# Optimization experiments

Hardware: AMD Instinct MI355X
Metric: run time of the kernel (lower is better)

Reference implementation:

```python
import jax, jax.numpy as jnp
import numpy as np

B, S, E = 2, 256, 512
H, DH = 8, 64            # heads, head_dim = E // H
TC = 768                 # tokens already resident in the paged cache


def setup_inputs() -> dict:
    key = jax.random.key(0)
    ks = jax.random.split(key, 8)
    scale = 1.0 / np.sqrt(E)
    return {
        "x": jax.random.normal(ks[0], (B, S, E), dtype=jnp.float32),
        # cache is stored token-major flattened over heads: [B, TC*H, DH]
        "k_cache": jax.random.normal(ks[1], (B, TC * H, DH), dtype=jnp.float32),
        "v_cache": jax.random.normal(ks[2], (B, TC * H, DH), dtype=jnp.float32),
        "Wq": jax.random.normal(ks[3], (E, E), dtype=jnp.float32) * scale,
        "bq": jnp.zeros((E,), dtype=jnp.float32),
        "Wk": jax.random.normal(ks[4], (E, E), dtype=jnp.float32) * scale,
        "bk": jnp.zeros((E,), dtype=jnp.float32),
        "Wv": jax.random.normal(ks[5], (E, E), dtype=jnp.float32) * scale,
        "bv": jnp.zeros((E,), dtype=jnp.float32),
        "Wo": jax.random.normal(ks[6], (E, E), dtype=jnp.float32) * scale,
        "bo": jnp.zeros((E,), dtype=jnp.float32),
    }


def reference(x, k_cache, v_cache, Wq, bq, Wk, bk, Wv, bv, Wo, bo):
    b, s, _ = x.shape
    # projections (torch Linear: y = x @ W.T + b)
    Q = (x @ Wq.T + bq).reshape(b, s, H, DH).transpose(0, 2, 1, 3)       # [B,H,S,DH]
    new_K = (x @ Wk.T + bk).reshape(b, s, H, DH)                         # [B,S,H,DH]
    new_V = (x @ Wv.T + bv).reshape(b, s, H, DH)
    # cache appends per-token [B,H,DH] slices and cats along dim=-2,
    # producing token-major flattened KV of shape [B, T*H, DH]
    K = jnp.concatenate([k_cache, new_K.reshape(b, s * H, DH)], axis=1)  # [B,L,DH]
    V = jnp.concatenate([v_cache, new_V.reshape(b, s * H, DH)], axis=1)
    # broadcasted matmul: Q [B,H,S,DH] against K [B,1,L,DH] -> scores [B,H,S,L]
    scores = jnp.einsum("bhsd,bld->bhsl", Q, K) / np.sqrt(DH).astype(jnp.float32)
    attn = jax.nn.softmax(scores, axis=-1)
    out = jnp.einsum("bhsl,bld->bhsd", attn, V)                          # [B,H,S,DH]
    out = out.transpose(0, 2, 1, 3).reshape(b, s, E)
    return out @ Wo.T + bo
```

## Files before the change

### kernel.cpp

```cpp
#include <hip/hip_runtime.h>
#include <math.h>

#define B_   2
#define LTOT   8192
#define LCACHE 6144
#define LNEW   2048

#define QSCALE (0.125f * 1.44269504088896f)

typedef __attribute__((ext_vector_type(8))) short bf16x8;
typedef __attribute__((ext_vector_type(4))) float f32x4;

__device__ __forceinline__ ushort f2bf(float f) {
    unsigned u = __float_as_uint(f);
    return (ushort)((u + 0x7fffu + ((u >> 16) & 1u)) >> 16);
}
__device__ __forceinline__ void split_hilo(float v, ushort& h, ushort& l) {
    h = f2bf(v);
    l = f2bf(v - __uint_as_float((unsigned)h << 16));
}


__device__ __forceinline__ void convert_slot(
    const float* __restrict__ src, ushort* __restrict__ dh, ushort* __restrict__ dl, int slot)
{
    const int R = slot >> 10, kk = (slot >> 6) & 15, ln = slot & 63;
    const int row = R * 16 + (ln & 15), col = kk * 32 + (ln >> 4) * 8;
    const float4 a  = *reinterpret_cast<const float4*>(src + row * 512 + col);
    const float4 b4 = *reinterpret_cast<const float4*>(src + row * 512 + col + 4);
    ushort4 h0, l0, h1, l1;
    split_hilo(a.x,  h0.x, l0.x); split_hilo(a.y,  h0.y, l0.y);
    split_hilo(a.z,  h0.z, l0.z); split_hilo(a.w,  h0.w, l0.w);
    split_hilo(b4.x, h1.x, l1.x); split_hilo(b4.y, h1.y, l1.y);
    split_hilo(b4.z, h1.z, l1.z); split_hilo(b4.w, h1.w, l1.w);
    *reinterpret_cast<ushort4*>(dh + slot * 8)     = h0;
    *reinterpret_cast<ushort4*>(dh + slot * 8 + 4) = h1;
    *reinterpret_cast<ushort4*>(dl + slot * 8)     = l0;
    *reinterpret_cast<ushort4*>(dl + slot * 8 + 4) = l1;
}

__device__ __forceinline__ void kcache_slot(
    const float* __restrict__ Kc, ushort* __restrict__ Khi, ushort* __restrict__ Klo,
    int b, int slot)
{
    const int key = slot >> 3, g = slot & 7;
    const int h = g >> 2, lg = g & 3;
    const float* src = Kc + ((size_t)b * LCACHE + key) * 64 + g * 8;
    const float4 a  = *reinterpret_cast<const float4*>(src);
    const float4 b4 = *reinterpret_cast<const float4*>(src + 4);
    const int T = key >> 5, r = key & 31;
    const int lr = ((r >> 3) << 2) | (r & 3), st = (r >> 2) & 1;
    const size_t dst = (size_t)b * 524288 + T * 2048 + st * 1024
                     + h * 512 + (((size_t)lg << 4 | lr)) * 8;
    ushort4 h0, l0, h1, l1;
    split_hilo(a.x,  h0.x, l0.x); split_hilo(a.y,  h0.y, l0.y);
    split_hilo(a.z,  h0.z, l0.z); split_hilo(a.w,  h0.w, l0.w);
    split_hilo(b4.x, h1.x, l1.x); split_hilo(b4.y, h1.y, l1.y);
    split_hilo(b4.z, h1.z, l1.z); split_hilo(b4.w, h1.w, l1.w);
    *reinterpret_cast<ushort4*>(Khi + dst)     = h0;
    *reinterpret_cast<ushort4*>(Khi + dst + 4) = h1;
    *reinterpret_cast<ushort4*>(Klo + dst)     = l0;
    *reinterpret_cast<ushort4*>(Klo + dst + 4) = l1;
}

__device__ __forceinline__ void proj8(
    const ushort* __restrict__ AhF, const ushort* __restrict__ AlF,
    const ushort* __restrict__ BhF, const ushort* __restrict__ BlF,
    const float* __restrict__ bias, const int mode, const int bxp, const int byp,
    ushort* __restrict__ d1, ushort* __restrict__ d2, float* __restrict__ df)
{
    const int tid = threadIdx.x;
    const int wv = tid >> 6, lane = tid & 63;
    const int lr = lane & 15, lg = lane >> 4;
    const int m0 = byp * 64 + (wv & 3) * 16;
    const int n0 = bxp * 64 + (wv >> 2) * 32;
    const int mT = m0 >> 4, nT = n0 >> 4;

    f32x4 acc[2];
    acc[0] = (f32x4){0.f, 0.f, 0.f, 0.f};
    acc[1] = (f32x4){0.f, 0.f, 0.f, 0.f};

    const ushort* Ah = AhF + (size_t)nT * 8192 + lane * 8;
    const ushort* Al = AlF + (size_t)nT * 8192 + lane * 8;
    const ushort* Bh = BhF + (size_t)mT * 8192 + lane * 8;
    const ushort* Bl = BlF + (size_t)mT * 8192 + lane * 8;

#pragma unroll 4
    for (int kk = 0; kk < 16; ++kk) {
        bf16x8 ah[2], al[2], bh, bl;
#pragma unroll
        for (int t = 0; t < 2; ++t) {
            ah[t] = *reinterpret_cast<const bf16x8*>(Ah + t * 8192 + kk * 512);
            al[t] = *reinterpret_cast<const bf16x8*>(Al + t * 8192 + kk * 512);
        }
        bh = *reinterpret_cast<const bf16x8*>(Bh + kk * 512);
        bl = *reinterpret_cast<const bf16x8*>(Bl + kk * 512);
        __builtin_amdgcn_s_setprio(1);
#pragma unroll
        for (int ni = 0; ni < 2; ++ni) {
            acc[ni] = __builtin_amdgcn_mfma_f32_16x16x32_bf16(ah[ni], bh, acc[ni], 0, 0, 0);
            acc[ni] = __builtin_amdgcn_mfma_f32_16x16x32_bf16(ah[ni], bl, acc[ni], 0, 0, 0);
            acc[ni] = __builtin_amdgcn_mfma_f32_16x16x32_bf16(al[ni], bh, acc[ni], 0, 0, 0);
        }
        __builtin_amdgcn_s_setprio(0);
    }

#pragma unroll
    for (int ni = 0; ni < 2; ++ni) {
        const int tok = m0 + lr;
        const int e   = n0 + ni * 16 + lg * 4;
        const float4 bb4 = *reinterpret_cast<const float4*>(&bias[e]);
        float v0 = acc[ni].x + bb4.x, v1 = acc[ni].y + bb4.y;
        float v2 = acc[ni].z + bb4.z, v3 = acc[ni].w + bb4.w;
        const int bb = tok >> 8, s = tok & 255;
        if (mode == 0) {
            v0 *= QSCALE; v1 *= QSCALE; v2 *= QSCALE; v3 *= QSCALE;
            ushort4 h, l;
            split_hilo(v0, h.x, l.x); split_hilo(v1, h.y, l.y);
            split_hilo(v2, h.z, l.z); split_hilo(v3, h.w, l.w);
            const size_t off = (size_t)bb * 131072 + s * 512 + e;
            *reinterpret_cast<ushort4*>(d1 + off) = h;
            *reinterpret_cast<ushort4*>(d2 + off) = l;
        } else if (mode == 1) {
            const int key = LCACHE + s * 8 + (e >> 6);
            const int d0 = e & 63;
            const int T = key >> 5, r = key & 31;
            const int klr = ((r >> 3) << 2) | (r & 3), st = (r >> 2) & 1;
            const int h = d0 >> 5, lg2 = (d0 >> 3) & 3, j0 = d0 & 7;
            const size_t dst = (size_t)bb * 524288 + T * 2048 + st * 1024
                             + h * 512 + ((lg2 << 4) | klr) * 8 + j0;
            ushort4 hh, ll;
            split_hilo(v0, hh.x, ll.x); split_hilo(v1, hh.y, ll.y);
            split_hilo(v2, hh.z, ll.z); split_hilo(v3, hh.w, ll.w);
            *reinterpret_cast<ushort4*>(d1 + dst) = hh;
            *reinterpret_cast<ushort4*>(d2 + dst) = ll;
        } else if (mode == 2) {
            const int key = LCACHE + s * 8 + (e >> 6);
            const int Tv = key >> 5;
            const int lg3 = (key & 31) >> 3, j = key & 7;
            const float vals[4] = {v0, v1, v2, v3};
#pragma unroll
            for (int c = 0; c < 4; ++c) {
                const int d = (e & 63) + c;
                const int dt = d >> 4, vlr = d & 15;
                d1[(size_t)bb * 524288 + Tv * 2048 + dt * 512
                   + ((lg3 << 4) | vlr) * 8 + j] = f2bf(vals[c]);
            }
        } else {
            float4 o; o.x = v0; o.y = v1; o.z = v2; o.w = v3;
            *reinterpret_cast<float4*>(df + (size_t)tok * 512 + e) = o;
        }
    }
}

#define ALOAD(kf, lf, vf, t) do {                                                   \
    _Pragma("unroll")                                                               \
    for (int st = 0; st < 2; ++st) {                                                \
        _Pragma("unroll")                                                           \
        for (int h = 0; h < 2; ++h) {                                               \
            kf[st][h] = *reinterpret_cast<const bf16x8*>(kh_p + (t) * 2048 + st * 1024 + h * 512); \
            lf[st][h] = *reinterpret_cast<const bf16x8*>(kl_p + (t) * 2048 + st * 1024 + h * 512); \
        }                                                                           \
    }                                                                               \
    _Pragma("unroll")                                                               \
    for (int dt = 0; dt < 4; ++dt)                                                  \
        vf[dt] = *reinterpret_cast<const bf16x8*>(vt_p + (t) * 2048 + dt * 512);    \
} while (0)

#define ACOMP(kf, lf, vf) do {                                                      \
    f32x4 s0 = {0.f,0.f,0.f,0.f}, s1 = {0.f,0.f,0.f,0.f};                           \
    __builtin_amdgcn_s_setprio(1);                                                  \
    _Pragma("unroll")                                                               \
    for (int h = 0; h < 2; ++h) {                                                   \
        s0 = __builtin_amdgcn_mfma_f32_16x16x32_bf16(kf[0][h], qh[h], s0, 0, 0, 0); \
        s0 = __builtin_amdgcn_mfma_f32_16x16x32_bf16(kf[0][h], ql[h], s0, 0, 0, 0); \
        s0 = __builtin_amdgcn_mfma_f32_16x16x32_bf16(lf[0][h], qh[h], s0, 0, 0, 0); \
        s1 = __builtin_amdgcn_mfma_f32_16x16x32_bf16(kf[1][h], qh[h], s1, 0, 0, 0); \
        s1 = __builtin_amdgcn_mfma_f32_16x16x32_bf16(kf[1][h], ql[h], s1, 0, 0, 0); \
        s1 = __builtin_amdgcn_mfma_f32_16x16x32_bf16(lf[1][h], qh[h], s1, 0, 0, 0); \
    }                                                                               \
    __builtin_amdgcn_s_setprio(0);                                                  \
    float tm = fmaxf(fmaxf(fmaxf(s0.x, s0.y), fmaxf(s0.z, s0.w)),                   \
                     fmaxf(fmaxf(s1.x, s1.y), fmaxf(s1.z, s1.w)));                  \
    tm = fmaxf(tm, __shfl_xor(tm, 16));                                             \
    tm = fmaxf(tm, __shfl_xor(tm, 32));                                             \
    const float mn = fmaxf(m, tm);                                                  \
    const float corr = __builtin_exp2f(m - mn);                                     \
    float p[8];                                                                     \
    p[0] = __builtin_exp2f(s0.x - mn); p[1] = __builtin_exp2f(s0.y - mn);           \
    p[2] = __builtin_exp2f(s0.z - mn); p[3] = __builtin_exp2f(s0.w - mn);           \
    p[4] = __builtin_exp2f(s1.x - mn); p[5] = __builtin_exp2f(s1.y - mn);           \
    p[6] = __builtin_exp2f(s1.z - mn); p[7] = __builtin_exp2f(s1.w - mn);           \
    float ps = ((p[0]+p[1]) + (p[2]+p[3])) + ((p[4]+p[5]) + (p[6]+p[7]));           \
    ps += __shfl_xor(ps, 16);                                                       \
    ps += __shfl_xor(ps, 32);                                                       \
    l = l * corr + ps; m = mn;                                                      \
    union { bf16x8 v; ushort u[8]; } pf;                                            \
    _Pragma("unroll")                                                               \
    for (int j = 0; j < 8; ++j) pf.u[j] = f2bf(p[j]);                               \
    __builtin_amdgcn_s_setprio(1);                                                  \
    _Pragma("unroll")                                                               \
    for (int dt = 0; dt < 4; ++dt) {                                                \
        f32x4 a = acc[dt];                                                          \
        a.x *= corr; a.y *= corr; a.z *= corr; a.w *= corr;                         \
        acc[dt] = __builtin_amdgcn_mfma_f32_16x16x32_bf16(vf[dt], pf.v, a, 0, 0, 0);\
    }                                                                               \
    __builtin_amdgcn_s_setprio(0);                                                  \
} while (0)

__device__ __forceinline__ void gridbarrier(uint* flags, uint* rel, int bar, int bid)
{
    __syncthreads();
    const uint ep = 0x1357A001u + (uint)bar;
    uint* f = flags + bar * 256;
    if (threadIdx.x == 0)
        __hip_atomic_store(f + bid, ep, __ATOMIC_RELEASE, __HIP_MEMORY_SCOPE_AGENT);
    if (bid == 0) {
        if (threadIdx.x < 256) {
            while (__hip_atomic_load(f + threadIdx.x, __ATOMIC_RELAXED,
                                     __HIP_MEMORY_SCOPE_AGENT) != ep)
                __builtin_amdgcn_s_sleep(32);
        }
        __syncthreads();
        if (threadIdx.x == 0)
            __hip_atomic_store(rel + bar, ep, __ATOMIC_RELEASE, __HIP_MEMORY_SCOPE_AGENT);
    }
    if (threadIdx.x == 0) {
        while (__hip_atomic_load(rel + bar, __ATOMIC_RELAXED,
                                 __HIP_MEMORY_SCOPE_AGENT) != ep)
            __builtin_amdgcn_s_sleep(32);
        (void)__hip_atomic_load(f + bid, __ATOMIC_ACQUIRE, __HIP_MEMORY_SCOPE_AGENT);
    }
    __syncthreads();
}

__global__ __launch_bounds__(512, 2) void fused_all(
    const float* __restrict__ x,  const float* __restrict__ Kc,
    const float* __restrict__ Vc,
    const float* __restrict__ Wq, const float* __restrict__ bq,
    const float* __restrict__ Wk, const float* __restrict__ bk,
    const float* __restrict__ Wv, const float* __restrict__ bv,
    const float* __restrict__ Wo, const float* __restrict__ bo,
    float* __restrict__ out,
    ushort* __restrict__ Khi, ushort* __restrict__ Klo, ushort* __restrict__ VtS,
    ushort* __restrict__ Qhi, ushort* __restrict__ Qlo,
    ushort* __restrict__ xh,  ushort* __restrict__ xl,
    ushort* __restrict__ Wqh, ushort* __restrict__ Wql,
    ushort* __restrict__ Wkh, ushort* __restrict__ Wkl,
    ushort* __restrict__ Wvh, ushort* __restrict__ Wvl,
    ushort* __restrict__ Woh, ushort* __restrict__ Wol,
    ushort* __restrict__ Aoh, ushort* __restrict__ Aol,
    uint* __restrict__ gflags, uint* __restrict__ grel)
{
    __shared__ union SM {
        ushort sT[64][68];
        struct { float sAcc[8][16][68]; float sM[8][16]; float sL[8][16]; } a;
    } sm;

    const int bid = blockIdx.x, tid = threadIdx.x;
    const int gid = bid * 512 + tid;

    {
        const int z = gid >> 15, slot = gid & 32767;
        const float* src; ushort* dh; ushort* dl;
        if (z == 0)      { src = x;  dh = xh;  dl = xl;  }
        else if (z == 1) { src = Wq; dh = Wqh; dl = Wql; }
        else if (z == 2) { src = Wk; dh = Wkh; dl = Wkl; }
        else             { src = Wv; dh = Wvh; dl = Wvl; }
        convert_slot(src, dh, dl, slot);
    }
    gridbarrier(gflags, grel, 0, bid);

    if (bid < 192) {
        const int z = bid >> 6, idx = bid & 63;
        const int bxp = idx & 7, byp = idx >> 3;
        if (z == 0)      proj8(Wqh, Wql, xh, xl, bq, 0, bxp, byp, Qhi, Qlo, nullptr);
        else if (z == 1) proj8(Wkh, Wkl, xh, xl, bk, 1, bxp, byp, Khi, Klo, nullptr);
        else             proj8(Wvh, Wvl, xh, xl, bv, 2, bxp, byp, VtS, nullptr, nullptr);
    } else {
        const int lid = (bid - 192) * 512 + tid;
        convert_slot(Wo, Woh, Wol, lid);
#pragma unroll
        for (int k = 0; k < 3; ++k) {
            int slot = lid + k * 32768;
            const int b = slot >= 49152 ? 1 : 0;
            kcache_slot(Kc, Khi, Klo, b, slot - b * 49152);
        }
#pragma unroll
        for (int vt = 0; vt < 3; ++vt) {
            const int tix = (bid - 192) * 3 + vt;
            const int b = tix / 96, kt = tix % 96;
            const int key0 = kt * 64;
            __syncthreads();
#pragma unroll
            for (int it = 0; it < 2; ++it) {
                const int id = it * 512 + tid;
                const int row = id >> 4, c4 = (id & 15) << 2;
                const float4 v = *reinterpret_cast<const float4*>(
                    &Vc[((size_t)b * LCACHE + key0 + row) * 64 + c4]);
                sm.sT[c4+0][row] = f2bf(v.x); sm.sT[c4+1][row] = f2bf(v.y);
                sm.sT[c4+2][row] = f2bf(v.z); sm.sT[c4+3][row] = f2bf(v.w);
            }
            __syncthreads();
            {
                const int s = tid;
                const int Tl = s >> 8, dt = (s >> 6) & 3, ln = s & 63;
                const int lr2 = ln & 15, lg2 = ln >> 4;
                const int kb = Tl * 32 + lg2 * 8;
                ushort4 o0, o1;
                o0.x = sm.sT[dt*16+lr2][kb+0]; o0.y = sm.sT[dt*16+lr2][kb+1];
                o0.z = sm.sT[dt*16+lr2][kb+2]; o0.w = sm.sT[dt*16+lr2][kb+3];
                o1.x = sm.sT[dt*16+lr2][kb+4]; o1.y = sm.sT[dt*16+lr2][kb+5];
                o1.z = sm.sT[dt*16+lr2][kb+6]; o1.w = sm.sT[dt*16+lr2][kb+7];
                const size_t dst = (size_t)b * 524288 + ((key0 >> 5) + Tl) * 2048
                                 + dt * 512 + ln * 8;
                *reinterpret_cast<ushort4*>(VtS + dst)     = o0;
                *reinterpret_cast<ushort4*>(VtS + dst + 4) = o1;
            }
        }
    }
    gridbarrier(gflags, grel, 1, bid);

    {
        const int wv = tid >> 6, lane = tid & 63;
        const int lr = lane & 15, lg = lane >> 4;
        const int xcd = bid & 7;
        const int b = xcd >> 2;
        const int qb = (bid >> 3) * 4 + (xcd & 3);

        bf16x8 qh[2], ql[2];
        {
            const int qrow0 = b * 2048 + qb * 16 + lr;
#pragma unroll
            for (int h = 0; h < 2; ++h) {
                const int off = qrow0 * 64 + h * 32 + lg * 8;
                qh[h] = *reinterpret_cast<const bf16x8*>(Qhi + off);
                ql[h] = *reinterpret_cast<const bf16x8*>(Qlo + off);
            }
        }

        const int T0 = wv * 32;
        const ushort* kh_p = Khi + (size_t)b * 524288 + (size_t)T0 * 2048 + lane * 8;
        const ushort* kl_p = Klo + (size_t)b * 524288 + (size_t)T0 * 2048 + lane * 8;
        const ushort* vt_p = VtS + (size_t)b * 524288 + (size_t)T0 * 2048 + lane * 8;

        f32x4 acc[4];
#pragma unroll
        for (int dt = 0; dt < 4; ++dt) acc[dt] = (f32x4){0.f, 0.f, 0.f, 0.f};
        float m = -INFINITY, l = 0.f;

        bf16x8 kfA[2][2], lfA[2][2], vfA[4];
        bf16x8 kfB[2][2], lfB[2][2], vfB[4];

        ALOAD(kfA, lfA, vfA, 0);
        for (int tt = 0; tt < 16; ++tt) {
            ALOAD(kfB, lfB, vfB, 2 * tt + 1);
            ACOMP(kfA, lfA, vfA);
            if (tt < 15) ALOAD(kfA, lfA, vfA, 2 * tt + 2);
            ACOMP(kfB, lfB, vfB);
        }

        __syncthreads();
#pragma unroll
        for (int dt = 0; dt < 4; ++dt) {
            float4 o; o.x = acc[dt].x; o.y = acc[dt].y; o.z = acc[dt].z; o.w = acc[dt].w;
            *reinterpret_cast<float4*>(&sm.a.sAcc[wv][lr][dt * 16 + lg * 4]) = o;
        }
        if (lg == 0) { sm.a.sM[wv][lr] = m; sm.a.sL[wv][lr] = l; }
        __syncthreads();

        {
            const int row = tid >> 5, d0 = (tid & 31) * 2;
            float ms = -INFINITY;
#pragma unroll
            for (int w = 0; w < 8; ++w) ms = fmaxf(ms, sm.a.sM[w][row]);
            float den = 0.f, n0 = 0.f, n1 = 0.f;
#pragma unroll
            for (int w = 0; w < 8; ++w) {
                const float e = __builtin_exp2f(sm.a.sM[w][row] - ms);
                den = fmaf(sm.a.sL[w][row], e, den);
                const float2 a = *reinterpret_cast<const float2*>(&sm.a.sAcc[w][row][d0]);
                n0 = fmaf(a.x, e, n0);
                n1 = fmaf(a.y, e, n1);
            }
            const float inv = 1.0f / den;
            const float v0 = n0 * inv, v1 = n1 * inv;
            const int row_g = b * 2048 + qb * 16 + row;
            const int qr = row_g & 2047;
            const int tok = b * 256 + (qr >> 3);
            const int e_  = (qr & 7) * 64 + d0;
            const int R = tok >> 4, lrr = tok & 15, kk = e_ >> 5, lgg = (e_ >> 3) & 3;
            const size_t dst = (size_t)R * 8192 + kk * 512 + ((lgg << 4) | lrr) * 8 + (d0 & 7);
            ushort h0, l0u, h1, l1u;
            split_hilo(v0, h0, l0u); split_hilo(v1, h1, l1u);
            ushort2 ho; ho.x = h0; ho.y = h1;
            ushort2 lo; lo.x = l0u; lo.y = l1u;
            *reinterpret_cast<ushort2*>(Aoh + dst) = ho;
            *reinterpret_cast<ushort2*>(Aol + dst) = lo;
        }
    }
    gridbarrier(gflags, grel, 2, bid);

    if (bid < 64) {
        const int bxp = bid & 7, byp = bid >> 3;
        proj8(Woh, Wol, Aoh, Aol, bo, 3, bxp, byp, nullptr, nullptr, out);
    }
}

extern "C" void kernel_launch(void* const* d_in, const int* in_sizes, int n_in,
                              void* d_out, int out_size, void* d_ws, size_t ws_size,
                              hipStream_t stream)
{
    const float* x  = (const float*)d_in[0];
    const float* kc = (const float*)d_in[1];
    const float* vc = (const float*)d_in[2];
    const float* Wq = (const float*)d_in[3];
    const float* bq = (const float*)d_in[4];
    const float* Wk = (const float*)d_in[5];
    const float* bk = (const float*)d_in[6];
    const float* Wv = (const float*)d_in[7];
    const float* bv = (const float*)d_in[8];
    const float* Wo = (const float*)d_in[9];
    const float* bo = (const float*)d_in[10];
    float* out = (float*)d_out;

    ushort* us  = (ushort*)d_ws;
    ushort* Khi = us;
    ushort* Klo = us + 1048576;
    ushort* VtS = us + 2097152;
    ushort* Qhi = us + 3145728;
    ushort* Qlo = us + 3407872;
    ushort* xh  = us + 3670016;
    ushort* xl  = us + 3932160;
    ushort* Wqh = us + 4194304;
    ushort* Wql = us + 4456448;
    ushort* Wkh = us + 4718592;
    ushort* Wkl = us + 4980736;
    ushort* Wvh = us + 5242880;
    ushort* Wvl = us + 5505024;
    ushort* Woh = us + 5767168;
    ushort* Wol = us + 6029312;
    ushort* Aoh = us + 6291456;
    ushort* Aol = us + 6553600;
    uint* gflags = (uint*)(us + 8388608);
    uint* grel   = gflags + 768;

    fused_all<<<dim3(256), dim3(512), 0, stream>>>(
        x, kc, vc, Wq, bq, Wk, bk, Wv, bv, Wo, bo, out,
        Khi, Klo, VtS, Qhi, Qlo, xh, xl,
        Wqh, Wql, Wkh, Wkl, Wvh, Wvl, Woh, Wol,
        Aoh, Aol, gflags, grel);
}
```

Baseline: 158.0 us.

## Split attention keys across blocks with global partial-softmax combine phase

The attention phase is remapped. Before, each block took 16 query rows, and its 8 waves each scanned a slice of the keys and combined in LDS. Now each block takes 128 query rows (one per wave), all against a single 1/8 key split, so the K/V data a block loads is shared by its 8 waves instead of every block streaming the whole key range. Per-split partial accumulators plus running max and sum go to global workspace, which reuses the dead x/W conversion buffers. A new grid barrier and a combine pass merge them and write the bf16 hi/lo attention output. The grid-barrier spin sleep is also shortened. The cost is extra global partial traffic and one more grid-wide barrier.

Result: slower. 172.6 us (+9.3%).

```diff
diff --git a/kernel.cpp b/kernel.cpp
--- a/kernel.cpp
+++ b/kernel.cpp
@@ -5,6 +5,7 @@
 #define LTOT   8192
 #define LCACHE 6144
 #define LNEW   2048
+#define NSPL   8
 
 #define QSCALE (0.125f * 1.44269504088896f)
 
@@ -219,7 +220,7 @@
         if (threadIdx.x < 256) {
             while (__hip_atomic_load(f + threadIdx.x, __ATOMIC_RELAXED,
                                      __HIP_MEMORY_SCOPE_AGENT) != ep)
-                __builtin_amdgcn_s_sleep(32);
+                __builtin_amdgcn_s_sleep(8);
         }
         __syncthreads();
         if (threadIdx.x == 0)
@@ -228,7 +229,7 @@
     if (threadIdx.x == 0) {
         while (__hip_atomic_load(rel + bar, __ATOMIC_RELAXED,
                                  __HIP_MEMORY_SCOPE_AGENT) != ep)
-            __builtin_amdgcn_s_sleep(32);
+            __builtin_amdgcn_s_sleep(8);
         (void)__hip_atomic_load(f + bid, __ATOMIC_ACQUIRE, __HIP_MEMORY_SCOPE_AGENT);
     }
     __syncthreads();
@@ -250,12 +251,11 @@
     ushort* __restrict__ Wvh, ushort* __restrict__ Wvl,
     ushort* __restrict__ Woh, ushort* __restrict__ Wol,
     ushort* __restrict__ Aoh, ushort* __restrict__ Aol,
+    float* __restrict__ PaccA, float* __restrict__ PaccB,
+    float* __restrict__ Pm, float* __restrict__ Pl,
     uint* __restrict__ gflags, uint* __restrict__ grel)
 {
-    __shared__ union SM {
-        ushort sT[64][68];
-        struct { float sAcc[8][16][68]; float sM[8][16]; float sL[8][16]; } a;
-    } sm;
+    __shared__ ushort sT[64][68];
 
     const int bid = blockIdx.x, tid = threadIdx.x;
     const int gid = bid * 512 + tid;
@@ -298,8 +298,8 @@
                 const int row = id >> 4, c4 = (id & 15) << 2;
                 const float4 v = *reinterpret_cast<const float4*>(
                     &Vc[((size_t)b * LCACHE + key0 + row) * 64 + c4]);
-                sm.sT[c4+0][row] = f2bf(v.x); sm.sT[c4+1][row] = f2bf(v.y);
-                sm.sT[c4+2][row] = f2bf(v.z); sm.sT[c4+3][row] = f2bf(v.w);
+                sT[c4+0][row] = f2bf(v.x); sT[c4+1][row] = f2bf(v.y);
+                sT[c4+2][row] = f2bf(v.z); sT[c4+3][row] = f2bf(v.w);
             }
             __syncthreads();
             {
@@ -308,10 +308,10 @@
                 const int lr2 = ln & 15, lg2 = ln >> 4;
                 const int kb = Tl * 32 + lg2 * 8;
                 ushort4 o0, o1;
-                o0.x = sm.sT[dt*16+lr2][kb+0]; o0.y = sm.sT[dt*16+lr2][kb+1];
-                o0.z = sm.sT[dt*16+lr2][kb+2]; o0.w = sm.sT[dt*16+lr2][kb+3];
-                o1.x = sm.sT[dt*16+lr2][kb+4]; o1.y = sm.sT[dt*16+lr2][kb+5];
-                o1.z = sm.sT[dt*16+lr2][kb+6]; o1.w = sm.sT[dt*16+lr2][kb+7];
+                o0.x = sT[dt*16+lr2][kb+0]; o0.y = sT[dt*16+lr2][kb+1];
+                o0.z = sT[dt*16+lr2][kb+2]; o0.w = sT[dt*16+lr2][kb+3];
+                o1.x = sT[dt*16+lr2][kb+4]; o1.y = sT[dt*16+lr2][kb+5];
+                o1.z = sT[dt*16+lr2][kb+6]; o1.w = sT[dt*16+lr2][kb+7];
                 const size_t dst = (size_t)b * 524288 + ((key0 >> 5) + Tl) * 2048
                                  + dt * 512 + ln * 8;
                 *reinterpret_cast<ushort4*>(VtS + dst)     = o0;
@@ -324,22 +324,20 @@
     {
         const int wv = tid >> 6, lane = tid & 63;
         const int lr = lane & 15, lg = lane >> 4;
-        const int xcd = bid & 7;
-        const int b = xcd >> 2;
-        const int qb = (bid >> 3) * 4 + (xcd & 3);
-
+        const int split = bid & 7;
+        const int b = (bid >> 3) & 1;
+        const int g = bid >> 4;
+
+        const int qrow = b * 2048 + g * 128 + wv * 16 + lr;
         bf16x8 qh[2], ql[2];
-        {
-            const int qrow0 = b * 2048 + qb * 16 + lr;
-#pragma unroll
-            for (int h = 0; h < 2; ++h) {
-                const int off = qrow0 * 64 + h * 32 + lg * 8;
-                qh[h] = *reinterpret_cast<const bf16x8*>(Qhi + off);
-                ql[h] = *reinterpret_cast<const bf16x8*>(Qlo + off);
-            }
-        }
-
-        const int T0 = wv * 32;
+#pragma unroll
+        for (int h = 0; h < 2; ++h) {
+            const int off = qrow * 64 + h * 32 + lg * 8;
+            qh[h] = *reinterpret_cast<const bf16x8*>(Qhi + off);
+            ql[h] = *reinterpret_cast<const bf16x8*>(Qlo + off);
+        }
+
+        const int T0 = split * 32;
         const ushort* kh_p = Khi + (size_t)b * 524288 + (size_t)T0 * 2048 + lane * 8;
         const ushort* kl_p = Klo + (size_t)b * 524288 + (size_t)T0 * 2048 + lane * 8;
         const ushort* vt_p = VtS + (size_t)b * 524288 + (size_t)T0 * 2048 + lane * 8;
@@ -360,46 +358,54 @@
             ACOMP(kfB, lfB, vfB);
         }
 
-        __syncthreads();
+        float* Pb = (split < 4) ? PaccA : PaccB;
+        float* dst = Pb + ((size_t)qrow * 4 + (split & 3)) * 64;
 #pragma unroll
         for (int dt = 0; dt < 4; ++dt) {
             float4 o; o.x = acc[dt].x; o.y = acc[dt].y; o.z = acc[dt].z; o.w = acc[dt].w;
-            *reinterpret_cast<float4*>(&sm.a.sAcc[wv][lr][dt * 16 + lg * 4]) = o;
-        }
-        if (lg == 0) { sm.a.sM[wv][lr] = m; sm.a.sL[wv][lr] = l; }
-        __syncthreads();
-
-        {
-            const int row = tid >> 5, d0 = (tid & 31) * 2;
-            float ms = -INFINITY;
-#pragma unroll
-            for (int w = 0; w < 8; ++w) ms = fmaxf(ms, sm.a.sM[w][row]);
-            float den = 0.f, n0 = 0.f, n1 = 0.f;
-#pragma unroll
-            for (int w = 0; w < 8; ++w) {
-                const float e = __builtin_exp2f(sm.a.sM[w][row] - ms);
-                den = fmaf(sm.a.sL[w][row], e, den);
-                const float2 a = *reinterpret_cast<const float2*>(&sm.a.sAcc[w][row][d0]);
-                n0 = fmaf(a.x, e, n0);
-                n1 = fmaf(a.y, e, n1);
-            }
-            const float inv = 1.0f / den;
-            const float v0 = n0 * inv, v1 = n1 * inv;
-            const int row_g = b * 2048 + qb * 16 + row;
-            const int qr = row_g & 2047;
-            const int tok = b * 256 + (qr >> 3);
-            const int e_  = (qr & 7) * 64 + d0;
-            const int R = tok >> 4, lrr = tok & 15, kk = e_ >> 5, lgg = (e_ >> 3) & 3;
-            const size_t dst = (size_t)R * 8192 + kk * 512 + ((lgg << 4) | lrr) * 8 + (d0 & 7);
-            ushort h0, l0u, h1, l1u;
-            split_hilo(v0, h0, l0u); split_hilo(v1, h1, l1u);
-            ushort2 ho; ho.x = h0; ho.y = h1;
-            ushort2 lo; lo.x = l0u; lo.y = l1u;
-            *reinterpret_cast<ushort2*>(Aoh + dst) = ho;
-            *reinterpret_cast<ushort2*>(Aol + dst) = lo;
+            *reinterpret_cast<float4*>(dst + dt * 16 + lg * 4) = o;
+        }
+        if (lg == 0) {
+            Pm[(size_t)qrow * NSPL + split] = m;
+            Pl[(size_t)qrow * NSPL + split] = l;
         }
     }
     gridbarrier(gflags, grel, 2, bid);
+
+    {
+        const int row = gid >> 5, d0 = (gid & 31) * 2;
+        float mv[NSPL], ms = -INFINITY;
+#pragma unroll
+        for (int sp = 0; sp < NSPL; ++sp) {
+            mv[sp] = Pm[row * NSPL + sp];
+            ms = fmaxf(ms, mv[sp]);
+        }
+        float den = 0.f, n0 = 0.f, n1 = 0.f;
+#pragma unroll
+        for (int sp = 0; sp < NSPL; ++sp) {
+            const float e = __builtin_exp2f(mv[sp] - ms);
+            den = fmaf(Pl[row * NSPL + sp], e, den);
+            const float* Pb = (sp < 4) ? PaccA : PaccB;
+            const float2 a = *reinterpret_cast<const float2*>(
+                &Pb[((size_t)row * 4 + (sp & 3)) * 64 + d0]);
+            n0 = fmaf(a.x, e, n0);
+            n1 = fmaf(a.y, e, n1);
+        }
+        const float inv = 1.0f / den;
+        const float v0 = n0 * inv, v1 = n1 * inv;
+        const int b = row >> 11, qr = row & 2047;
+        const int tok = b * 256 + (qr >> 3);
+        const int e_  = (qr & 7) * 64 + d0;
+        const int R = tok >> 4, lrr = tok & 15, kk = e_ >> 5, lgg = (e_ >> 3) & 3;
+        const size_t dst = (size_t)R * 8192 + kk * 512 + ((lgg << 4) | lrr) * 8 + (d0 & 7);
+        ushort h0, l0u, h1, l1u;
+        split_hilo(v0, h0, l0u); split_hilo(v1, h1, l1u);
+        ushort2 ho; ho.x = h0; ho.y = h1;
+        ushort2 lo; lo.x = l0u; lo.y = l1u;
+        *reinterpret_cast<ushort2*>(Aoh + dst) = ho;
+        *reinterpret_cast<ushort2*>(Aol + dst) = lo;
+    }
+    gridbarrier(gflags, grel, 3, bid);
 
     if (bid < 64) {
         const int bxp = bid & 7, byp = bid >> 3;
@@ -442,12 +448,19 @@
     ushort* Wol = us + 6029312;
     ushort* Aoh = us + 6291456;
     ushort* Aol = us + 6553600;
-    uint* gflags = (uint*)(us + 8388608);
-    uint* grel   = gflags + 768;
+
+    float* PaccA = (float*)(us + 3670016);
+    float* PaccB = (float*)((char*)d_ws + 13631488);
+    float* Pm    = (float*)((char*)d_ws + 17825792);
+    float* Pl    = (float*)((char*)d_ws + 17956864);
+    uint*  gflags = (uint*)((char*)d_ws + 18087936);
+    uint*  grel   = gflags + 1024;
+
+    (void)ws_size; (void)in_sizes; (void)n_in; (void)out_size;
 
     fused_all<<<dim3(256), dim3(512), 0, stream>>>(
         x, kc, vc, Wq, bq, Wk, bk, Wv, bv, Wo, bo, out,
         Khi, Klo, VtS, Qhi, Qlo, xh, xl,
         Wqh, Wql, Wkh, Wkl, Wvh, Wvl, Woh, Wol,
-        Aoh, Aol, gflags, grel);
-}
+        Aoh, Aol, PaccA, PaccB, Pm, Pl, gflags, grel);
+}
```
